# Kernel optimization log

Measured on AMD Instinct MI355X. Metric: run time of the kernel, lower is better.

The kernel has to match this reference:

```python
import jax, jax.numpy as jnp
import numpy as np
from jax import lax

SEQ, BATCH, IN, HID, LAYERS = 1024, 64, 384, 384, 5


def setup_inputs() -> dict:
    key = jax.random.key(0)
    kx, kw, kb = jax.random.split(key, 3)
    x = jax.random.normal(kx, (SEQ, BATCH, IN), dtype=jnp.float32)
    # Each QRNN layer (window=1): Linear(in, 3*hidden). in == hidden == 384 for all layers.
    scale = 1.0 / np.sqrt(IN)
    Ws = jax.random.uniform(kw, (LAYERS, IN, 3 * HID), dtype=jnp.float32, minval=-scale, maxval=scale)
    bs = jax.random.uniform(kb, (LAYERS, 3 * HID), dtype=jnp.float32, minval=-scale, maxval=scale)
    return {"x": x, "Ws": Ws, "bs": bs}


def _fo_pool(F, Z):
    # c_t = F_t * Z_t + (1 - F_t) * c_{t-1}, c_0 = 0  (ForgetMult, hidden=None)
    # linear recurrence c_t = a_t * c_{t-1} + b_t solved with associative scan over time.
    a = 1.0 - F
    b = F * Z
    def comb(l, r):
        a1, b1 = l
        a2, b2 = r
        return a2 * a1, a2 * b1 + b2
    _, C = lax.associative_scan(comb, (a, b), axis=0)
    return C


def _qrnn_layer(h, W, b):
    Y = jnp.einsum('sbi,ij->sbj', h, W) + b  # (S, B, 3H)
    Z, F, O = jnp.split(Y, 3, axis=-1)
    Z = jnp.tanh(Z)
    F = jax.nn.sigmoid(F)
    C = _fo_pool(F, Z)
    return jax.nn.sigmoid(O) * C


def reference(x, Ws, bs):
    h = x
    for i in range(LAYERS):
        h = _qrnn_layer(h, Ws[i], bs[i])
    return h
```

## Files before the change

kernel.cpp:

```cpp
#include <hip/hip_runtime.h>
#include <hip/hip_bf16.h>
#include <stdint.h>

#define SEQ    1024
#define BATCH  64
#define DIN    384
#define HID    384
#define NLAYER 5

constexpr int Ncols = 3 * HID;
constexpr int Kdim  = DIN;

typedef __attribute__((ext_vector_type(8))) __bf16 bf16x8;
typedef __attribute__((ext_vector_type(4))) float  f32x4;
typedef unsigned int u32;
typedef uint16_t u16;

__device__ __forceinline__ u16 f32_to_bf16_rn(float x) {
  u32 u = __float_as_uint(x);
  u += 0x7FFFu + ((u >> 16) & 1u);
  return (u16)(u >> 16);
}
__device__ __forceinline__ float bf16_to_f32(u16 h) {
  return __uint_as_float(((u32)h) << 16);
}
__device__ __forceinline__ float bflo(u32 p) { return __uint_as_float(p << 16); }
__device__ __forceinline__ float bfhi(u32 p) { return __uint_as_float(p & 0xFFFF0000u); }
__device__ __forceinline__ u32 packbf(float a, float b) {
  return (u32)f32_to_bf16_rn(a) | ((u32)f32_to_bf16_rn(b) << 16);
}
__device__ __forceinline__ void split2(float x, u16& hi, u16& lo) {
  u16 h = f32_to_bf16_rn(x);
  lo = f32_to_bf16_rn(x - bf16_to_f32(h));
  hi = h;
}

__device__ __forceinline__ void gload_lds16(const void* g, void* l) {
  __builtin_amdgcn_global_load_lds(
      (const __attribute__((address_space(1))) void*)g,
      (__attribute__((address_space(3))) void*)l, 16, 0, 0);
}

__device__ __forceinline__ int jmap(int jp) {
  if (jp >= 768) return jp;
  const int w = jp & 31;
  return ((jp >> 5) << 4) + (w & 15) + ((w & 16) ? 384 : 0);
}

__global__ void k_prep_w(const float* __restrict__ W, u16* __restrict__ wthi,
                         u16* __restrict__ wtlo) {
  __shared__ float tile[64][65];
  const int n0 = blockIdx.x * 64;
  const int k0 = blockIdx.y * 64;
  const int layer = blockIdx.z;
  const float* Wl = W + (size_t)layer * Kdim * Ncols;
  const int tx = threadIdx.x & 63, ty = threadIdx.x >> 6;
  const int jsrc = jmap(n0 + tx);
  #pragma unroll
  for (int i = 0; i < 64; i += 4)
    tile[ty + i][tx] = Wl[(size_t)(k0 + ty + i) * Ncols + jsrc];
  __syncthreads();
  u16* whl = wthi + (size_t)layer * Ncols * Kdim;
  u16* wll = wtlo + (size_t)layer * Ncols * Kdim;
  #pragma unroll
  for (int i = 0; i < 64; i += 4) {
    const int n = n0 + ty + i, k = k0 + tx;
    u16 hi, lo; split2(tile[tx][ty + i], hi, lo);
    whl[(size_t)n * Kdim + k] = hi;
    wll[(size_t)n * Kdim + k] = lo;
  }
}

__global__ void k_prep_xg(const float* __restrict__ x, u32* __restrict__ ap,
                          int n8, int bgRow) {
  int i = blockIdx.x * blockDim.x + threadIdx.x;
  const int stride = gridDim.x * blockDim.x;
  const float4* x4 = (const float4*)x;
  for (; i < n8; i += stride) {
    const int rl = i / 48;
    const int k8 = i - rl * 48;
    const int b_local = rl >> 10, s = rl & 1023;
    const size_t src = (size_t)(s * 64 + bgRow + b_local) * 96 + k8 * 2;
    const float4 v0 = x4[src], v1 = x4[src + 1];
    uint4 o;
    o.x = packbf(v0.x, v0.y); o.y = packbf(v0.z, v0.w);
    o.z = packbf(v1.x, v1.y); o.w = packbf(v1.z, v1.w);
    ((uint4*)ap)[i] = o;
  }
}

__global__ __launch_bounds__(256, 3) void k_gemm(
    const u16* __restrict__ A,
    const u16* __restrict__ Whi, const u16* __restrict__ Wlo,
    const float* __restrict__ bias,
    u32* __restrict__ zf, u32* __restrict__ ov,
    float* __restrict__ compA, float* __restrict__ compB,
    int Mtiles, int NCHg)
{
  __shared__ char smem[49152];
  char* sA  = smem;
  char* sWh = smem + 16384;
  char* sWl = smem + 32768;

  const int tid  = threadIdx.x;
  const int L = blockIdx.y * 9 + blockIdx.x;
  const int q = (9 * Mtiles) >> 3;
  const int nl = (L & 7) * q + (L >> 3);
  const int mt = nl / 9;
  const int n0 = (nl - mt * 9) * 128;
  const int m0 = mt * 128;

  const int wave = tid >> 6, lane = tid & 63;

  f32x4 acc[8][2] = {};

  const int sr   = tid >> 3;
  const int sseg = tid & 7;

  for (int kt = 0; kt < Kdim / 64; ++kt) {
    const int k0 = kt * 64;
    __syncthreads();
    #pragma unroll
    for (int i = 0; i < 4; ++i) {
      const int r = i * 32 + sr;
      const int seg = sseg ^ (r & 7);
      const size_t ea = (size_t)(m0 + r) * Kdim + k0 + seg * 8;
      const size_t eb = (size_t)(n0 + r) * Kdim + k0 + seg * 8;
      const u32 loff = (u32)r * 128 + sseg * 16;
      gload_lds16(A + ea,   sA  + loff);
      gload_lds16(Whi + eb, sWh + loff);
      gload_lds16(Wlo + eb, sWl + loff);
    }
    __syncthreads();
    #pragma unroll
    for (int ks = 0; ks < 2; ++ks) {
      const int cbase = ks * 4 + (lane >> 4);
      bf16x8 fA[8], fh[2], fl[2];
      #pragma unroll
      for (int m = 0; m < 8; ++m) {
        const int row = m * 16 + (lane & 15);
        const u32 off = (u32)row * 128 + ((cbase ^ (row & 7)) * 16);
        fA[m] = *(const bf16x8*)(sA + off);
      }
      #pragma unroll
      for (int n = 0; n < 2; ++n) {
        const int row = wave * 32 + n * 16 + (lane & 15);
        const u32 off = (u32)row * 128 + ((cbase ^ (row & 7)) * 16);
        fh[n] = *(const bf16x8*)(sWh + off);
        fl[n] = *(const bf16x8*)(sWl + off);
      }
      #pragma unroll
      for (int m = 0; m < 8; ++m)
        #pragma unroll
        for (int n = 0; n < 2; ++n) {
          acc[m][n] = __builtin_amdgcn_mfma_f32_16x16x32_bf16(fA[m], fh[n], acc[m][n], 0, 0, 0);
          acc[m][n] = __builtin_amdgcn_mfma_f32_16x16x32_bf16(fA[m], fl[n], acc[m][n], 0, 0, 0);
        }
    }
  }

  const int qv = lane >> 4;
  const int ln = lane & 15;

  if (n0 < 768) {
    const int hcol = (n0 >> 1) + wave * 16 + ln;
    const float bz = bias[hcol];
    const float bf = bias[384 + hcol];
    float Arun = 1.f, Brun = 0.f;
    #pragma unroll
    for (int m = 0; m < 8; ++m) {
      float Aseg = 1.f, Bseg = 0.f;
      #pragma unroll
      for (int r = 0; r < 4; ++r) {
        float vz = acc[m][0][r] + bz;
        float vf = acc[m][1][r] + bf;
        vz = fminf(30.f, fmaxf(-30.f, vz));
        vf = fminf(30.f, fmaxf(-30.f, vf));
        const float sz = 1.f / (1.f + __expf(-2.f * vz));
        const float z  = fmaf(2.f, sz, -1.f);
        const float f  = 1.f / (1.f + __expf(-vf));
        const float av = 1.f - f;
        const float bb = f * z;
        const int row = m * 16 + qv * 4 + r;
        zf[(size_t)(m0 + row) * 384 + hcol] = packbf(av, bb);
        Bseg = fmaf(av, Bseg, bb);
        Aseg *= av;
      }
      {
        const float Ao = __shfl_xor(Aseg, 16), Bo = __shfl_xor(Bseg, 16);
        const bool late = qv & 1;
        const float Ae = late ? Ao : Aseg, Be = late ? Bo : Bseg;
        const float Al = late ? Aseg : Ao, Bl = late ? Bseg : Bo;
        Aseg = Al * Ae; Bseg = fmaf(Al, Be, Bl);
      }
      {
        const float Ao = __shfl_xor(Aseg, 32), Bo = __shfl_xor(Bseg, 32);
        const bool late = (qv >> 1) & 1;
        const float Ae = late ? Ao : Aseg, Be = late ? Bo : Bseg;
        const float Al = late ? Aseg : Ao, Bl = late ? Bseg : Bo;
        Aseg = Al * Ae; Bseg = fmaf(Al, Be, Bl);
      }
      Brun = fmaf(Aseg, Brun, Bseg);
      Arun *= Aseg;
    }
    if (qv == 0) {
      const int b_local = mt >> 3, chunk = mt & 7;
      const int chg = b_local * 384 + hcol;
      compA[chunk * NCHg + chg] = Arun;
      compB[chunk * NCHg + chg] = Brun;
    }
  } else {
    const int hb = (n0 - 768) + wave * 32 + ln;
    const float b0 = bias[768 + hb];
    const float b1 = bias[768 + hb + 16];
    const int pos = ((hb >> 5) << 4) + (hb & 15);
    #pragma unroll
    for (int m = 0; m < 8; ++m)
      #pragma unroll
      for (int r = 0; r < 4; ++r) {
        float v0 = acc[m][0][r] + b0;
        float v1 = acc[m][1][r] + b1;
        v0 = fminf(30.f, fmaxf(-30.f, v0));
        v1 = fminf(30.f, fmaxf(-30.f, v1));
        const float s0 = 1.f / (1.f + __expf(-v0));
        const float s1 = 1.f / (1.f + __expf(-v1));
        const int row = m * 16 + qv * 4 + r;
        ov[(size_t)(m0 + row) * 192 + pos] = packbf(s0, s1);
      }
  }
}

template<int WM>
__global__ void k_scan(const u32* __restrict__ zfp, const u32* __restrict__ op,
                       const float* __restrict__ compA, const float* __restrict__ compB,
                       u32* __restrict__ anext, float* __restrict__ out,
                       int NCHg, int bgRow)
{
  const int ch = blockIdx.x * blockDim.x + threadIdx.x;
  if (ch >= NCHg) return;
  const int chunk = blockIdx.y;
  const int b_local = ch / 384;
  const int h = ch - b_local * 384;
  float c = 0.f;
  for (int q = 0; q < chunk; ++q)
    c = fmaf(compA[q * NCHg + ch], c, compB[q * NCHg + ch]);

  const int r0 = b_local * 1024 + chunk * 128;
  const size_t zbase = (size_t)r0 * 384 + h;
  const size_t obase = (size_t)r0 * 192 + (((h >> 5) << 4) + (h & 15));
  const int osel = (h >> 4) & 1;

  u32 ab0[8], ab1[8], ow0[8], ow1[8];
  #pragma unroll
  for (int u = 0; u < 8; ++u) {
    ab0[u] = zfp[zbase + (size_t)u * 384];
    ow0[u] = op[obase + (size_t)u * 192];
  }
  for (int t0 = 0; t0 < 128; t0 += 16) {
    const size_t zb = zbase + (size_t)t0 * 384;
    const size_t ob = obase + (size_t)t0 * 192;
    #pragma unroll
    for (int u = 0; u < 8; ++u) {
      ab1[u] = zfp[zb + (size_t)(u + 8) * 384];
      ow1[u] = op[ob + (size_t)(u + 8) * 192];
    }
    #pragma unroll
    for (int u = 0; u < 8; ++u) {
      c = fmaf(bflo(ab0[u]), c, bfhi(ab0[u]));
      const float o = osel ? bfhi(ow0[u]) : bflo(ow0[u]);
      const float hv = o * c;
      const int t = t0 + u;
      if (WM == 0) {
        const u32 me = (u32)f32_to_bf16_rn(hv);
        const u32 nb = (u32)__shfl_xor((int)me, 1);
        if (!(h & 1)) anext[(size_t)(r0 + t) * 192 + (h >> 1)] = me | (nb << 16);
      } else {
        out[(size_t)((chunk * 128 + t) * 64 + bgRow + b_local) * 384 + h] = hv;
      }
    }
    if (t0 + 16 < 128) {
      #pragma unroll
      for (int u = 0; u < 8; ++u) {
        ab0[u] = zfp[zb + (size_t)(u + 16) * 384];
        ow0[u] = op[ob + (size_t)(u + 16) * 192];
      }
    }
    #pragma unroll
    for (int u = 0; u < 8; ++u) {
      c = fmaf(bflo(ab1[u]), c, bfhi(ab1[u]));
      const float o = osel ? bfhi(ow1[u]) : bflo(ow1[u]);
      const float hv = o * c;
      const int t = t0 + u + 8;
      if (WM == 0) {
        const u32 me = (u32)f32_to_bf16_rn(hv);
        const u32 nb = (u32)__shfl_xor((int)me, 1);
        if (!(h & 1)) anext[(size_t)(r0 + t) * 192 + (h >> 1)] = me | (nb << 16);
      } else {
        out[(size_t)((chunk * 128 + t) * 64 + bgRow + b_local) * 384 + h] = hv;
      }
    }
  }
}

extern "C" void kernel_launch(void* const* d_in, const int* in_sizes, int n_in,
                              void* d_out, int out_size, void* d_ws, size_t ws_size,
                              hipStream_t stream) {
  const float* x  = (const float*)d_in[0];
  const float* Ws = (const float*)d_in[1];
  const float* bs = (const float*)d_in[2];
  float* out = (float*)d_out;

  const size_t wbytes = (size_t)NLAYER * Ncols * Kdim * 2;
  int G = 64;
  for (int g = 1; g <= 64; g *= 2) {
    const int Bg_ = BATCH / g;
    const size_t MG_ = (size_t)SEQ * Bg_;
    size_t need = 2 * wbytes
                + MG_ * Kdim * 2
                + MG_ * 384 * 4
                + MG_ * 192 * 4
                + 2 * (size_t)8 * Bg_ * 384 * 4
                + 16 * 256;
    if (need <= ws_size) { G = g; break; }
  }
  const int Bg = BATCH / G;
  const int MG = SEQ * Bg;
  const int NCHg = Bg * HID;
  const int Mtiles = MG / 128;

  char* p = (char*)d_ws;
  auto carve = [&](size_t bytes) -> char* {
    char* r = p; p += (bytes + 255) & ~(size_t)255; return r;
  };
  u16* Whi = (u16*)carve(wbytes);
  u16* Wlo = (u16*)carve(wbytes);
  u32* Ap  = (u32*)carve((size_t)MG * Kdim * 2);
  u32* zf  = (u32*)carve((size_t)MG * 384 * 4);
  u32* ov  = (u32*)carve((size_t)MG * 192 * 4);
  float* cA = (float*)carve((size_t)8 * NCHg * 4);
  float* cB = (float*)carve((size_t)8 * NCHg * 4);

  k_prep_w<<<dim3(Ncols / 64, Kdim / 64, NLAYER), 256, 0, stream>>>(Ws, Whi, Wlo);

  const int scanBlocks = (NCHg + 255) / 256;
  for (int bg = 0; bg < G; ++bg) {
    const int bgRow = bg * Bg;
    const int n8 = MG * (Kdim / 8);
    const int pblocks = (n8 + 255) / 256 < 4096 ? (n8 + 255) / 256 : 4096;
    k_prep_xg<<<pblocks, 256, 0, stream>>>(x, Ap, n8, bgRow);

    for (int layer = 0; layer < NLAYER; ++layer) {
      const u16* wh = Whi + (size_t)layer * Ncols * Kdim;
      const u16* wl = Wlo + (size_t)layer * Ncols * Kdim;
      const float* bias = bs + layer * Ncols;
      k_gemm<<<dim3(9, Mtiles), 256, 0, stream>>>(
          (const u16*)Ap, wh, wl, bias, zf, ov, cA, cB, Mtiles, NCHg);
      if (layer < NLAYER - 1)
        k_scan<0><<<dim3(scanBlocks, 8), 256, 0, stream>>>(
            zf, ov, cA, cB, Ap, out, NCHg, bgRow);
      else
        k_scan<1><<<dim3(scanBlocks, 8), 256, 0, stream>>>(
            zf, ov, cA, cB, Ap, out, NCHg, bgRow);
    }
  }
}
```

Measured before the change: 943.0 us.

## Pre-swizzle weights into MFMA fragment order and load them directly to registers

The weight prep kernel now writes the hi/lo bf16 split weights in per-lane MFMA fragment order, so the GEMM loads B operands straight from global memory into registers instead of staging them through LDS. A tiles are double-buffered in LDS, with the next k-step's A and W fragments prefetched while the current step computes, leaving one barrier per step. Bias is folded into the accumulator initialisation, the clamps are removed, and division is replaced by hardware reciprocal. LDS use drops, but register pressure rises and launch bounds fall from 3 to 2 blocks per CU, which lowers occupancy.

```diff
diff --git a/kernel.cpp b/kernel.cpp
--- a/kernel.cpp
+++ b/kernel.cpp
@@ -16,6 +16,8 @@
 typedef unsigned int u32;
 typedef uint16_t u16;
 
+constexpr int WF_U4_PER_LAYER = 9 * 4 * 6 * 8 * 64;
+
 __device__ __forceinline__ u16 f32_to_bf16_rn(float x) {
   u32 u = __float_as_uint(x);
   u += 0x7FFFu + ((u >> 16) & 1u);
@@ -41,33 +43,45 @@
       (__attribute__((address_space(3))) void*)l, 16, 0, 0);
 }
 
-__device__ __forceinline__ int jmap(int jp) {
-  if (jp >= 768) return jp;
-  const int w = jp & 31;
-  return ((jp >> 5) << 4) + (w & 15) + ((w & 16) ? 384 : 0);
-}
-
-__global__ void k_prep_w(const float* __restrict__ W, u16* __restrict__ wthi,
-                         u16* __restrict__ wtlo) {
-  __shared__ float tile[64][65];
-  const int n0 = blockIdx.x * 64;
-  const int k0 = blockIdx.y * 64;
+__global__ void k_prep_w(const float* __restrict__ W, uint4* __restrict__ wf) {
+  __shared__ float lds[64][130];
+  const int nt = blockIdx.x;
+  const int kt = blockIdx.y;
   const int layer = blockIdx.z;
-  const float* Wl = W + (size_t)layer * Kdim * Ncols;
-  const int tx = threadIdx.x & 63, ty = threadIdx.x >> 6;
-  const int jsrc = jmap(n0 + tx);
-  #pragma unroll
-  for (int i = 0; i < 64; i += 4)
-    tile[ty + i][tx] = Wl[(size_t)(k0 + ty + i) * Ncols + jsrc];
+  const float* Wl = W + (size_t)layer * Kdim * Ncols + (size_t)kt * 64 * Ncols;
+  const int tid = threadIdx.x;
+  for (int e = tid; e < 64 * 128; e += 256) {
+    const int kl = e >> 7, jj = e & 127;
+    int j;
+    if (nt < 6) j = (jj < 64) ? (nt * 64 + jj) : (384 + nt * 64 + jj - 64);
+    else        j = 768 + (nt - 6) * 128 + jj;
+    lds[kl][jj] = Wl[(size_t)kl * Ncols + j];
+  }
   __syncthreads();
-  u16* whl = wthi + (size_t)layer * Ncols * Kdim;
-  u16* wll = wtlo + (size_t)layer * Ncols * Kdim;
-  #pragma unroll
-  for (int i = 0; i < 64; i += 4) {
-    const int n = n0 + ty + i, k = k0 + tx;
-    u16 hi, lo; split2(tile[tx][ty + i], hi, lo);
-    whl[(size_t)n * Kdim + k] = hi;
-    wll[(size_t)n * Kdim + k] = lo;
+  #pragma unroll
+  for (int i = 0; i < 8; ++i) {
+    const int cid = i * 256 + tid;
+    const int ws = cid >> 9;
+    const int rem = cid & 511;
+    const int c = rem >> 6;
+    const int lane = rem & 63;
+    const int ks = c >> 2, pl = (c >> 1) & 1, n = c & 1;
+    int jj;
+    if (nt < 6) jj = ws * 16 + (lane & 15) + (n ? 64 : 0);
+    else        jj = ws * 32 + n * 16 + (lane & 15);
+    const int kl = ks * 32 + (lane >> 4) * 8;
+    u16 h[8];
+    #pragma unroll
+    for (int t = 0; t < 8; ++t) {
+      u16 hi, lo; split2(lds[kl + t][jj], hi, lo);
+      h[t] = pl ? lo : hi;
+    }
+    uint4 o;
+    o.x = (u32)h[0] | ((u32)h[1] << 16);
+    o.y = (u32)h[2] | ((u32)h[3] << 16);
+    o.z = (u32)h[4] | ((u32)h[5] << 16);
+    o.w = (u32)h[6] | ((u32)h[7] << 16);
+    wf[((((size_t)layer * 9 + nt) * 4 + ws) * 48 + kt * 8 + c) * 64 + lane] = o;
   }
 }
 
@@ -89,96 +103,111 @@
   }
 }
 
-__global__ __launch_bounds__(256, 3) void k_gemm(
+__global__ __launch_bounds__(256, 2) void k_gemm(
     const u16* __restrict__ A,
-    const u16* __restrict__ Whi, const u16* __restrict__ Wlo,
+    const bf16x8* __restrict__ Wf,
     const float* __restrict__ bias,
     u32* __restrict__ zf, u32* __restrict__ ov,
     float* __restrict__ compA, float* __restrict__ compB,
     int Mtiles, int NCHg)
 {
-  __shared__ char smem[49152];
-  char* sA  = smem;
-  char* sWh = smem + 16384;
-  char* sWl = smem + 32768;
+  __shared__ char smem[32768];
 
   const int tid  = threadIdx.x;
   const int L = blockIdx.y * 9 + blockIdx.x;
   const int q = (9 * Mtiles) >> 3;
   const int nl = (L & 7) * q + (L >> 3);
   const int mt = nl / 9;
-  const int n0 = (nl - mt * 9) * 128;
+  const int nt = nl - mt * 9;
   const int m0 = mt * 128;
 
   const int wave = tid >> 6, lane = tid & 63;
-
-  f32x4 acc[8][2] = {};
+  const int qv = lane >> 4;
+  const int ln = lane & 15;
+
+  float b0i, b1i;
+  if (nt < 6) {
+    const int hcol = nt * 64 + wave * 16 + ln;
+    b0i = bias[hcol];
+    b1i = bias[384 + hcol];
+  } else {
+    const int hb = (nt - 6) * 128 + wave * 32 + ln;
+    b0i = bias[768 + hb];
+    b1i = bias[768 + hb + 16];
+  }
+  f32x4 acc[8][2];
+  #pragma unroll
+  for (int m = 0; m < 8; ++m) {
+    acc[m][0] = f32x4{b0i, b0i, b0i, b0i};
+    acc[m][1] = f32x4{b1i, b1i, b1i, b1i};
+  }
 
   const int sr   = tid >> 3;
   const int sseg = tid & 7;
-
-  for (int kt = 0; kt < Kdim / 64; ++kt) {
-    const int k0 = kt * 64;
-    __syncthreads();
+  u32 abase[2];
+  #pragma unroll
+  for (int ks = 0; ks < 2; ++ks)
+    abase[ks] = (u32)(ln * 128 + (((ks * 4 + qv) ^ (ln & 7)) * 16));
+  const bf16x8* wbase = Wf + ((size_t)(nt * 4 + wave) * 48) * 64 + lane;
+
+  bf16x8 Wcur[8], Wnxt[8];
+
+  auto stageA = [&](int kt, int p) {
     #pragma unroll
     for (int i = 0; i < 4; ++i) {
       const int r = i * 32 + sr;
       const int seg = sseg ^ (r & 7);
-      const size_t ea = (size_t)(m0 + r) * Kdim + k0 + seg * 8;
-      const size_t eb = (size_t)(n0 + r) * Kdim + k0 + seg * 8;
-      const u32 loff = (u32)r * 128 + sseg * 16;
-      gload_lds16(A + ea,   sA  + loff);
-      gload_lds16(Whi + eb, sWh + loff);
-      gload_lds16(Wlo + eb, sWl + loff);
-    }
-    __syncthreads();
+      const size_t ea = (size_t)(m0 + r) * Kdim + kt * 64 + seg * 8;
+      gload_lds16(A + ea, smem + p * 16384 + r * 128 + sseg * 16);
+    }
+  };
+
+  stageA(0, 0);
+  #pragma unroll
+  for (int c = 0; c < 8; ++c) Wcur[c] = wbase[c * 64];
+  __syncthreads();
+
+  #pragma unroll
+  for (int kt = 0; kt < 6; ++kt) {
+    const int p = kt & 1;
+    if (kt < 5) {
+      stageA(kt + 1, p ^ 1);
+      #pragma unroll
+      for (int c = 0; c < 8; ++c) Wnxt[c] = wbase[((kt + 1) * 8 + c) * 64];
+    }
     #pragma unroll
     for (int ks = 0; ks < 2; ++ks) {
-      const int cbase = ks * 4 + (lane >> 4);
-      bf16x8 fA[8], fh[2], fl[2];
+      bf16x8 fA[8];
+      #pragma unroll
+      for (int m = 0; m < 8; ++m)
+        fA[m] = *(const bf16x8*)(smem + p * 16384 + m * 2048 + abase[ks]);
       #pragma unroll
       for (int m = 0; m < 8; ++m) {
-        const int row = m * 16 + (lane & 15);
-        const u32 off = (u32)row * 128 + ((cbase ^ (row & 7)) * 16);
-        fA[m] = *(const bf16x8*)(sA + off);
-      }
-      #pragma unroll
-      for (int n = 0; n < 2; ++n) {
-        const int row = wave * 32 + n * 16 + (lane & 15);
-        const u32 off = (u32)row * 128 + ((cbase ^ (row & 7)) * 16);
-        fh[n] = *(const bf16x8*)(sWh + off);
-        fl[n] = *(const bf16x8*)(sWl + off);
-      }
-      #pragma unroll
-      for (int m = 0; m < 8; ++m)
-        #pragma unroll
-        for (int n = 0; n < 2; ++n) {
-          acc[m][n] = __builtin_amdgcn_mfma_f32_16x16x32_bf16(fA[m], fh[n], acc[m][n], 0, 0, 0);
-          acc[m][n] = __builtin_amdgcn_mfma_f32_16x16x32_bf16(fA[m], fl[n], acc[m][n], 0, 0, 0);
-        }
-    }
-  }
-
-  const int qv = lane >> 4;
-  const int ln = lane & 15;
-
-  if (n0 < 768) {
-    const int hcol = (n0 >> 1) + wave * 16 + ln;
-    const float bz = bias[hcol];
-    const float bf = bias[384 + hcol];
+        acc[m][0] = __builtin_amdgcn_mfma_f32_16x16x32_bf16(fA[m], Wcur[ks * 4 + 0], acc[m][0], 0, 0, 0);
+        acc[m][1] = __builtin_amdgcn_mfma_f32_16x16x32_bf16(fA[m], Wcur[ks * 4 + 1], acc[m][1], 0, 0, 0);
+        acc[m][0] = __builtin_amdgcn_mfma_f32_16x16x32_bf16(fA[m], Wcur[ks * 4 + 2], acc[m][0], 0, 0, 0);
+        acc[m][1] = __builtin_amdgcn_mfma_f32_16x16x32_bf16(fA[m], Wcur[ks * 4 + 3], acc[m][1], 0, 0, 0);
+      }
+    }
+    if (kt < 5) {
+      __syncthreads();
+      #pragma unroll
+      for (int c = 0; c < 8; ++c) Wcur[c] = Wnxt[c];
+    }
+  }
+
+  if (nt < 6) {
+    const int hcol = nt * 64 + wave * 16 + ln;
     float Arun = 1.f, Brun = 0.f;
     #pragma unroll
     for (int m = 0; m < 8; ++m) {
       float Aseg = 1.f, Bseg = 0.f;
       #pragma unroll
       for (int r = 0; r < 4; ++r) {
-        float vz = acc[m][0][r] + bz;
-        float vf = acc[m][1][r] + bf;
-        vz = fminf(30.f, fmaxf(-30.f, vz));
-        vf = fminf(30.f, fmaxf(-30.f, vf));
-        const float sz = 1.f / (1.f + __expf(-2.f * vz));
-        const float z  = fmaf(2.f, sz, -1.f);
-        const float f  = 1.f / (1.f + __expf(-vf));
+        const float vz = acc[m][0][r];
+        const float vf = acc[m][1][r];
+        const float z = fmaf(2.f, __builtin_amdgcn_rcpf(1.f + __expf(-2.f * vz)), -1.f);
+        const float f = __builtin_amdgcn_rcpf(1.f + __expf(-vf));
         const float av = 1.f - f;
         const float bb = f * z;
         const int row = m * 16 + qv * 4 + r;
@@ -210,20 +239,14 @@
       compB[chunk * NCHg + chg] = Brun;
     }
   } else {
-    const int hb = (n0 - 768) + wave * 32 + ln;
-    const float b0 = bias[768 + hb];
-    const float b1 = bias[768 + hb + 16];
+    const int hb = (nt - 6) * 128 + wave * 32 + ln;
     const int pos = ((hb >> 5) << 4) + (hb & 15);
     #pragma unroll
     for (int m = 0; m < 8; ++m)
       #pragma unroll
       for (int r = 0; r < 4; ++r) {
-        float v0 = acc[m][0][r] + b0;
-        float v1 = acc[m][1][r] + b1;
-        v0 = fminf(30.f, fmaxf(-30.f, v0));
-        v1 = fminf(30.f, fmaxf(-30.f, v1));
-        const float s0 = 1.f / (1.f + __expf(-v0));
-        const float s1 = 1.f / (1.f + __expf(-v1));
+        const float s0 = __builtin_amdgcn_rcpf(1.f + __expf(-acc[m][0][r]));
+        const float s1 = __builtin_amdgcn_rcpf(1.f + __expf(-acc[m][1][r]));
         const int row = m * 16 + qv * 4 + r;
         ov[(size_t)(m0 + row) * 192 + pos] = packbf(s0, s1);
       }
@@ -310,12 +333,12 @@
   const float* bs = (const float*)d_in[2];
   float* out = (float*)d_out;
 
-  const size_t wbytes = (size_t)NLAYER * Ncols * Kdim * 2;
+  const size_t wfbytes = (size_t)NLAYER * WF_U4_PER_LAYER * 16;
   int G = 64;
   for (int g = 1; g <= 64; g *= 2) {
     const int Bg_ = BATCH / g;
     const size_t MG_ = (size_t)SEQ * Bg_;
-    size_t need = 2 * wbytes
+    size_t need = wfbytes
                 + MG_ * Kdim * 2
                 + MG_ * 384 * 4
                 + MG_ * 192 * 4
@@ -332,15 +355,14 @@
   auto carve = [&](size_t bytes) -> char* {
     char* r = p; p += (bytes + 255) & ~(size_t)255; return r;
   };
-  u16* Whi = (u16*)carve(wbytes);
-  u16* Wlo = (u16*)carve(wbytes);
+  uint4* Wf = (uint4*)carve(wfbytes);
   u32* Ap  = (u32*)carve((size_t)MG * Kdim * 2);
   u32* zf  = (u32*)carve((size_t)MG * 384 * 4);
   u32* ov  = (u32*)carve((size_t)MG * 192 * 4);
   float* cA = (float*)carve((size_t)8 * NCHg * 4);
   float* cB = (float*)carve((size_t)8 * NCHg * 4);
 
-  k_prep_w<<<dim3(Ncols / 64, Kdim / 64, NLAYER), 256, 0, stream>>>(Ws, Whi, Wlo);
+  k_prep_w<<<dim3(9, 6, NLAYER), 256, 0, stream>>>(Ws, Wf);
 
   const int scanBlocks = (NCHg + 255) / 256;
   for (int bg = 0; bg < G; ++bg) {
@@ -350,11 +372,10 @@
     k_prep_xg<<<pblocks, 256, 0, stream>>>(x, Ap, n8, bgRow);
 
     for (int layer = 0; layer < NLAYER; ++layer) {
-      const u16* wh = Whi + (size_t)layer * Ncols * Kdim;
-      const u16* wl = Wlo + (size_t)layer * Ncols * Kdim;
+      const bf16x8* wl = (const bf16x8*)(Wf + (size_t)layer * WF_U4_PER_LAYER);
       const float* bias = bs + layer * Ncols;
       k_gemm<<<dim3(9, Mtiles), 256, 0, stream>>>(
-          (const u16*)Ap, wh, wl, bias, zf, ov, cA, cB, Mtiles, NCHg);
+          (const u16*)Ap, wl, bias, zf, ov, cA, cB, Mtiles, NCHg);
       if (layer < NLAYER - 1)
         k_scan<0><<<dim3(scanBlocks, 8), 256, 0, stream>>>(
             zf, ov, cA, cB, Ap, out, NCHg, bgRow);
```

New measurement: 868.9 us. -7.9%, faster.
